# Optimization experiments

Hardware: AMD Instinct MI355X
Metric: run time of the kernel (lower is better)

## Reference

```python
import jax, jax.numpy as jnp
import numpy as np

N = 100000   # nodes
E = 800000   # edges
IN = 256     # input feature dim
H = 4        # heads per layer
D = 32       # per-head hidden dim (num_hidden)
SLOPE = 0.2  # leaky_relu negative slope


def setup_inputs() -> dict:
    key = jax.random.key(0)
    ks = jax.random.split(key, 8)
    s = 0.1  # weight scale for numerical stability
    x = jax.random.normal(ks[0], (N, IN), jnp.float32)
    edge_index = jax.random.randint(ks[1], (2, E), 0, N, dtype=jnp.int32)
    W0 = jax.random.normal(ks[2], (IN, H * D), jnp.float32) * s
    al0 = jax.random.normal(ks[3], (H, D), jnp.float32) * s
    ar0 = jax.random.normal(ks[4], (H, D), jnp.float32) * s
    W1 = jax.random.normal(ks[5], (H * D, H * D), jnp.float32) * s
    al1 = jax.random.normal(ks[6], (H, D), jnp.float32) * s
    ar1 = jax.random.normal(ks[7], (H, D), jnp.float32) * s
    return {"x": x, "edge_index": edge_index, "W0": W0, "al0": al0,
            "ar0": ar0, "W1": W1, "al1": al1, "ar1": ar1}


def _gat_layer(h, W, al, ar, src, dst, residual):
    """One GATConv: project, edge attention, dst-wise softmax, scatter-agg."""
    n = h.shape[0]
    feat = (h @ W).reshape(n, H, D)              # [N,H,D]
    el = jnp.einsum('nhd,hd->nh', feat, al)      # [N,H]
    er = jnp.einsum('nhd,hd->nh', feat, ar)      # [N,H]
    e = jax.nn.leaky_relu(el[src] + er[dst], SLOPE)   # raw scores [E,H]
    # edge softmax grouped by destination node (numerically stable)
    emax = jax.ops.segment_max(e, dst, num_segments=n)   # [N,H]
    eexp = jnp.exp(e - emax[dst])                          # [E,H]
    denom = jax.ops.segment_sum(eexp, dst, num_segments=n)  # [N,H]
    a = eexp / denom[dst]                                  # attention [E,H]
    msg = feat[src] * a[:, :, None]                        # [E,H,D]
    rst = jax.ops.segment_sum(msg, dst, num_segments=n)    # [N,H,D]
    if residual:
        rst = rst + h.reshape(n, H, D)  # identity residual (dims match)
    rst = jax.nn.elu(rst)               # activation
    return rst, a, e


def reference(x, edge_index, W0, al0, ar0, W1, al1, ar1):
    src, dst = edge_index[0], edge_index[1]
    # layer 0: no residual
    h1, a0, e0 = _gat_layer(x, W0, al0, ar0, src, dst, residual=False)
    atten0 = e0.mean(axis=-1)  # e_gat.flatten(1).mean(-1) -> [E]
    # layer 1: residual
    h2, a1, e1 = _gat_layer(h1.reshape(N, H * D), W1, al1, ar1, src, dst,
                            residual=True)
    atten1 = e1.mean(axis=-1)
    temp = h2.reshape(N, H * D)          # flattened node embeddings
    heads = tuple(h2[:, i] for i in range(H))  # per-head [N,D]
    return (temp,) + heads + (e1, atten0, atten1)
```

## Files before the change

### kernel.cpp

```cpp
#include <hip/hip_runtime.h>
#include <hip/hip_bf16.h>


typedef _Float16 f16;
typedef _Float16 f16x2 __attribute__((ext_vector_type(2)));
typedef _Float16 f16x8 __attribute__((ext_vector_type(8)));
typedef float f32x2 __attribute__((ext_vector_type(2)));
typedef float f32x4 __attribute__((ext_vector_type(4)));

__device__ __forceinline__ void gload16(const void* g, void* l) {
    __builtin_amdgcn_global_load_lds(
        (const __attribute__((address_space(1))) unsigned int*)g,
        (__attribute__((address_space(3))) unsigned int*)l, 16, 0, 0);
}

__global__ void prep(const float* __restrict__ W0, const float* __restrict__ W1,
                     f16* __restrict__ Wth0, f16* __restrict__ Wtl0,
                     f16* __restrict__ Wth1, f16* __restrict__ Wtl1,
                     const int* __restrict__ dsts, int* __restrict__ deg, int E) {
    int i = blockIdx.x * blockDim.x + threadIdx.x;
    if (i < 256 * 128) {
        int k = i >> 7, c = i & 127;
        float v = W0[i];
        f16 h = (f16)v;
        Wth0[(size_t)c * 256 + k] = h;
        Wtl0[(size_t)c * 256 + k] = (f16)(v - (float)h);
    } else if (i < 256 * 128 + 128 * 128) {
        int j = i - 256 * 128;
        int k = j >> 7, c = j & 127;
        float v = W1[j];
        f16 h = (f16)v;
        Wth1[(size_t)c * 128 + k] = h;
        Wtl1[(size_t)c * 128 + k] = (f16)(v - (float)h);
    } else {
        int e = i - (256 * 128 + 128 * 128);
        if (e < E) atomicAdd(&deg[dsts[e]], 1);
    }
}

template <int AFP16>
__device__ __forceinline__ void gemm_body(
        int bid, const void* __restrict__ Xv, const f16* __restrict__ Wth,
        const f16* __restrict__ Wtl, f16* __restrict__ Y16,
        const float* __restrict__ al, const float* __restrict__ ar,
        float* __restrict__ el_out, float* __restrict__ er_out,
        int nrows, int K) {
    __shared__ float As32[AFP16 ? 1 : 128 * 32];
    __shared__ f16   As16[AFP16 ? 128 * 32 : 1];
    __shared__ f16   Bh[128 * 32];
    __shared__ f16   Bl[128 * 32];
    const int t    = threadIdx.x;
    const int wave = t >> 6;
    const int lane = t & 63;
    const int lr   = lane & 15;
    const int kg   = lane >> 4;
    const int row0 = bid * 128;

    f32x4 acc[2][8];
    #pragma unroll
    for (int i = 0; i < 2; ++i)
        #pragma unroll
        for (int j = 0; j < 8; ++j) acc[i][j] = (f32x4){0.f, 0.f, 0.f, 0.f};

    for (int k0 = 0; k0 < K; k0 += 32) {
        if constexpr (!AFP16) {
            #pragma unroll
            for (int j = 0; j < 4; ++j) {
                int G = t + 256 * j;
                int row = G >> 3, slot = G & 7;
                int g = slot ^ (row & 7);
                int grow = row0 + row; if (grow >= nrows) grow = nrows - 1;
                gload16((const float*)Xv + (size_t)grow * K + k0 + g * 4,
                        &As32[G * 4]);
            }
        } else {
            #pragma unroll
            for (int j = 0; j < 2; ++j) {
                int G = t + 256 * j;
                int row = G >> 2, g4 = G & 3;
                int grow = row0 + row; if (grow >= nrows) grow = nrows - 1;
                gload16((const f16*)Xv + (size_t)grow * K + k0 + g4 * 8,
                        &As16[G * 8]);
            }
        }
        #pragma unroll
        for (int j = 0; j < 2; ++j) {
            int G = t + 256 * j;
            int r = G >> 2, g4 = G & 3;
            int p = ((r & 15) << 3) | (r >> 4);
            gload16(Wth + (size_t)p * K + k0 + g4 * 8, &Bh[G * 8]);
            gload16(Wtl + (size_t)p * K + k0 + g4 * 8, &Bl[G * 8]);
        }
        __syncthreads();

        const int ar0_ = wave * 32 + lr;
        f16x8 ah0, ah1, alo0, alo1;
        if constexpr (!AFP16) {
            int s0 = (2 * kg) ^ (lr & 7);
            int s1 = (2 * kg + 1) ^ (lr & 7);
            f32x4 u0 = *(const f32x4*)&As32[ar0_ * 32 + s0 * 4];
            f32x4 u1 = *(const f32x4*)&As32[ar0_ * 32 + s1 * 4];
            f32x4 v0 = *(const f32x4*)&As32[(ar0_ + 16) * 32 + s0 * 4];
            f32x4 v1 = *(const f32x4*)&As32[(ar0_ + 16) * 32 + s1 * 4];
            float a8[8] = {u0[0], u0[1], u0[2], u0[3], u1[0], u1[1], u1[2], u1[3]};
            float b8[8] = {v0[0], v0[1], v0[2], v0[3], v1[0], v1[1], v1[2], v1[3]};
            #pragma unroll
            for (int i = 0; i < 8; ++i) {
                f16 h0 = (f16)a8[i]; ah0[i] = h0; alo0[i] = (f16)(a8[i] - (float)h0);
                f16 h1 = (f16)b8[i]; ah1[i] = h1; alo1[i] = (f16)(b8[i] - (float)h1);
            }
        } else {
            ah0 = *(const f16x8*)&As16[ar0_ * 32 + kg * 8];
            ah1 = *(const f16x8*)&As16[(ar0_ + 16) * 32 + kg * 8];
        }
        f16x8 bh[8];
        #pragma unroll
        for (int cb = 0; cb < 8; ++cb)
            bh[cb] = *(const f16x8*)&Bh[(cb * 16 + lr) * 32 + kg * 8];

        #pragma unroll
        for (int cb = 0; cb < 8; ++cb) {
            acc[0][cb] = __builtin_amdgcn_mfma_f32_16x16x32_f16(ah0, bh[cb], acc[0][cb], 0, 0, 0);
            acc[1][cb] = __builtin_amdgcn_mfma_f32_16x16x32_f16(ah1, bh[cb], acc[1][cb], 0, 0, 0);
        }
        if constexpr (!AFP16) {
            #pragma unroll
            for (int cb = 0; cb < 8; ++cb) {
                acc[0][cb] = __builtin_amdgcn_mfma_f32_16x16x32_f16(alo0, bh[cb], acc[0][cb], 0, 0, 0);
                acc[1][cb] = __builtin_amdgcn_mfma_f32_16x16x32_f16(alo1, bh[cb], acc[1][cb], 0, 0, 0);
            }
        }
        #pragma unroll
        for (int cb = 0; cb < 8; ++cb) {
            f16x8 bl = *(const f16x8*)&Bl[(cb * 16 + lr) * 32 + kg * 8];
            acc[0][cb] = __builtin_amdgcn_mfma_f32_16x16x32_f16(ah0, bl, acc[0][cb], 0, 0, 0);
            acc[1][cb] = __builtin_amdgcn_mfma_f32_16x16x32_f16(ah1, bl, acc[1][cb], 0, 0, 0);
        }
        __syncthreads();
    }

    const int hh = lr >> 2;
    const int co = (lr & 3) * 8;
    float alv[8], arv[8];
    #pragma unroll
    for (int j = 0; j < 8; ++j) {
        alv[j] = al[hh * 32 + co + j];
        arv[j] = ar[hh * 32 + co + j];
    }
    #pragma unroll
    for (int rb = 0; rb < 2; ++rb) {
        int rbase = row0 + wave * 32 + rb * 16 + kg * 4;
        #pragma unroll
        for (int r = 0; r < 4; ++r) {
            int grow = rbase + r;
            f16x8 hv;
            float sl_ = 0.0f, sr_ = 0.0f;
            #pragma unroll
            for (int cb = 0; cb < 8; ++cb) {
                float v = acc[rb][cb][r];
                hv[cb] = (f16)v;
                sl_ += v * alv[cb];
                sr_ += v * arv[cb];
            }
            sl_ += __shfl_xor(sl_, 1); sl_ += __shfl_xor(sl_, 2);
            sr_ += __shfl_xor(sr_, 1); sr_ += __shfl_xor(sr_, 2);
            if (grow < nrows) {
                *(f16x8*)(Y16 + (size_t)grow * 128 + lr * 8) = hv;
                if ((lane & 3) == 0) {
                    el_out[4 * (size_t)grow + hh] = sl_;
                    er_out[4 * (size_t)grow + hh] = sr_;
                }
            }
        }
    }
}

__device__ __forceinline__ void scan_body(int b, const int* __restrict__ deg,
                                          int* __restrict__ excl,
                                          int* __restrict__ bsums, int n) {
    __shared__ int wsums[4];
    int t = threadIdx.x;
    int base = b * 1024;
    int idx = base + t * 4;
    int v[4];
    #pragma unroll
    for (int i = 0; i < 4; ++i) v[i] = (idx + i < n) ? deg[idx + i] : 0;
    int tsum = v[0] + v[1] + v[2] + v[3];
    int lane = t & 63, wid = t >> 6;
    int incl = tsum;
    #pragma unroll
    for (int off = 1; off < 64; off <<= 1) {
        int u = __shfl_up(incl, off, 64);
        if (lane >= off) incl += u;
    }
    if (lane == 63) wsums[wid] = incl;
    __syncthreads();
    if (t == 0) {
        int s = 0;
        #pragma unroll
        for (int w = 0; w < 4; ++w) { int x = wsums[w]; wsums[w] = s; s += x; }
    }
    __syncthreads();
    int ex = incl - tsum + wsums[wid];
    int run = ex;
    #pragma unroll
    for (int i = 0; i < 4; ++i) { if (idx + i < n) excl[idx + i] = run; run += v[i]; }
    if (t == 255) bsums[b] = ex + tsum;
}

__global__ __launch_bounds__(256, 2) void gemm0_scan(
        const float* __restrict__ X, const f16* __restrict__ Wth,
        const f16* __restrict__ Wtl, f16* __restrict__ Y16,
        const float* __restrict__ al, const float* __restrict__ ar,
        float* __restrict__ el_out, float* __restrict__ er_out,
        int nrows, int K, int gblocks,
        const int* __restrict__ deg, int* __restrict__ excl,
        int* __restrict__ bsums, int n) {
    if ((int)blockIdx.x < gblocks)
        gemm_body<0>(blockIdx.x, X, Wth, Wtl, Y16, al, ar, el_out, er_out, nrows, K);
    else
        scan_body(blockIdx.x - gblocks, deg, excl, bsums, n);
}

__global__ __launch_bounds__(256, 2) void gemm_mfma1(
        const f16* __restrict__ X, const f16* __restrict__ Wth,
        const f16* __restrict__ Wtl, f16* __restrict__ Y16,
        const float* __restrict__ al, const float* __restrict__ ar,
        float* __restrict__ el_out, float* __restrict__ er_out,
        int nrows, int K) {
    gemm_body<1>(blockIdx.x, X, Wth, Wtl, Y16, al, ar, el_out, er_out, nrows, K);
}

__global__ __launch_bounds__(256) void scan_fin(int* __restrict__ row_off,
                                                const int* __restrict__ bsums,
                                                int* __restrict__ cursor,
                                                const int* __restrict__ deg,
                                                int n, int nb) {
    __shared__ int spfx;
    int b = blockIdx.x;
    int t = threadIdx.x;
    if (t < 64) {
        int v = 0;
        if (t < b && t < nb) v = bsums[t];
        int t2 = t + 64;
        if (t2 < b && t2 < nb) v += bsums[t2];
        #pragma unroll
        for (int off = 32; off; off >>= 1) v += __shfl_xor(v, off, 64);
        if (t == 0) spfx = v;
    }
    __syncthreads();
    int pfx = spfx;
    int base = b * 1024 + t * 4;
    #pragma unroll
    for (int i2 = 0; i2 < 4; ++i2) {
        int i = base + i2;
        if (i < n) {
            int v = row_off[i] + pfx;
            row_off[i] = v;
            cursor[i]  = v;
            if (i == n - 1) row_off[n] = v + deg[i];
        }
    }
}

__global__ void fill_csr_edge0(const int* __restrict__ srcs, const int* __restrict__ dsts,
                               int* __restrict__ cursor, int* __restrict__ csr_src,
                               const float* __restrict__ el, const float* __restrict__ er,
                               float* __restrict__ atten0, int E) {
    int e = blockIdx.x * blockDim.x + threadIdx.x;
    if (e >= E) return;
    int s = srcs[e], d = dsts[e];
    int p = atomicAdd(&cursor[d], 1);
    csr_src[p] = s;
    float4 elv = *(const float4*)(el + 4 * (size_t)s);
    float4 erv = *(const float4*)(er + 4 * (size_t)d);
    float v0 = elv.x + erv.x, v1 = elv.y + erv.y;
    float v2 = elv.z + erv.z, v3 = elv.w + erv.w;
    v0 = v0 > 0.0f ? v0 : 0.2f * v0;
    v1 = v1 > 0.0f ? v1 : 0.2f * v1;
    v2 = v2 > 0.0f ? v2 : 0.2f * v2;
    v3 = v3 > 0.0f ? v3 : 0.2f * v3;
    __builtin_nontemporal_store((v0 + v1 + v2 + v3) * 0.25f, atten0 + e);
}

__device__ __forceinline__ void edge1_body(int bid,
        const int* __restrict__ srcs, const int* __restrict__ dsts,
        const float* __restrict__ el, const float* __restrict__ er,
        float* __restrict__ e1_out, float* __restrict__ atten1, int E) {
    int e = bid * 256 + threadIdx.x;
    if (e >= E) return;
    int s = srcs[e], d = dsts[e];
    float4 elv = *(const float4*)(el + 4 * (size_t)s);
    float4 erv = *(const float4*)(er + 4 * (size_t)d);
    float v0 = elv.x + erv.x, v1 = elv.y + erv.y;
    float v2 = elv.z + erv.z, v3 = elv.w + erv.w;
    v0 = v0 > 0.0f ? v0 : 0.2f * v0;
    v1 = v1 > 0.0f ? v1 : 0.2f * v1;
    v2 = v2 > 0.0f ? v2 : 0.2f * v2;
    v3 = v3 > 0.0f ? v3 : 0.2f * v3;
    __builtin_nontemporal_store((f32x4){v0, v1, v2, v3},
                                (f32x4*)(e1_out + 4 * (size_t)e));
    __builtin_nontemporal_store((v0 + v1 + v2 + v3) * 0.25f, atten1 + e);
}

template <int LAYER>
__device__ __forceinline__ void agg_body(int bid,
        const int* __restrict__ row_off, const int* __restrict__ csr_src,
        const float* __restrict__ el, const float* __restrict__ er,
        const f16* __restrict__ feat16, const f16* __restrict__ resid16,
        f16* __restrict__ out16, float* __restrict__ out32,
        float* __restrict__ heads, int N) {
    int wave = (bid * 256 + (int)threadIdx.x) >> 6;
    if (wave >= N) return;
    int lane = threadIdx.x & 63;
    int q  = lane >> 4;
    int sc = lane & 15;
    int h  = sc >> 2;
    int start = row_off[wave];
    int dc    = row_off[wave + 1] - start;
    float er_h = er[4 * (size_t)wave + h];

    float acc[8];
    #pragma unroll
    for (int j = 0; j < 8; ++j) acc[j] = 0.0f;
    float dh = 0.0f;

    for (int cs = 0; cs < dc; cs += 64) {
        int act = dc - cs; if (act > 64) act = 64;
        int sl = (lane < act) ? csr_src[start + cs + lane] : 0;
        int i = 0;
        for (; i + 8 <= act; i += 8) {
            int s0 = __shfl(sl, i + q);
            int s1 = __shfl(sl, i + 4 + q);
            float x0 = el[4 * (size_t)s0 + h] + er_h;
            float x1 = el[4 * (size_t)s1 + h] + er_h;
            x0 = x0 > 0.0f ? x0 : 0.2f * x0;
            x1 = x1 > 0.0f ? x1 : 0.2f * x1;
            float w0 = __expf(x0);
            float w1 = __expf(x1);
            f16x8 f0 = *(const f16x8*)(feat16 + 128 * (size_t)s0 + sc * 8);
            f16x8 f1 = *(const f16x8*)(feat16 + 128 * (size_t)s1 + sc * 8);
            #pragma unroll
            for (int j = 0; j < 8; ++j) acc[j] += w0 * (float)f0[j];
            #pragma unroll
            for (int j = 0; j < 8; ++j) acc[j] += w1 * (float)f1[j];
            dh += w0 + w1;
        }
        for (; i < act; i += 4) {
            int e = i + q;
            bool on = e < act;
            int s = __shfl(sl, on ? e : 0);
            float x = el[4 * (size_t)s + h] + er_h;
            x = x > 0.0f ? x : 0.2f * x;
            float w = on ? __expf(x) : 0.0f;
            f16x8 fv = *(const f16x8*)(feat16 + 128 * (size_t)s + sc * 8);
            #pragma unroll
            for (int j = 0; j < 8; ++j) acc[j] += w * (float)fv[j];
            dh += w;
        }
    }

    #pragma unroll
    for (int j = 0; j < 8; ++j) {
        acc[j] += __shfl_xor(acc[j], 16);
        acc[j] += __shfl_xor(acc[j], 32);
    }
    dh += __shfl_xor(dh, 16);
    dh += __shfl_xor(dh, 32);

    float inv = (dc > 0) ? 1.0f / dh : 0.0f;
    float ax = (q == 0) ? acc[0] : (q == 1) ? acc[2] : (q == 2) ? acc[4] : acc[6];
    float ay = (q == 0) ? acc[1] : (q == 1) ? acc[3] : (q == 2) ? acc[5] : acc[7];
    ax *= inv; ay *= inv;
    int c0 = sc * 8 + q * 2;
    size_t o = 128 * (size_t)wave + c0;
    if (LAYER == 1) {
        f16x2 rv = *(const f16x2*)(resid16 + o);
        ax += (float)rv[0]; ay += (float)rv[1];
    }
    ax = ax > 0.0f ? ax : __expf(ax) - 1.0f;
    ay = ay > 0.0f ? ay : __expf(ay) - 1.0f;
    if (LAYER == 0) {
        f16x2 hv; hv[0] = (f16)ax; hv[1] = (f16)ay;
        *(f16x2*)(out16 + o) = hv;
    } else {
        __builtin_nontemporal_store((f32x2){ax, ay}, (f32x2*)(out32 + o));
        __builtin_nontemporal_store(
            (f32x2){ax, ay},
            (f32x2*)(heads + (size_t)h * N * 32 + (size_t)wave * 32 + (c0 & 31)));
    }
}

__global__ __launch_bounds__(256) void aggregate0(const int* __restrict__ row_off,
                                                  const int* __restrict__ csr_src,
                                                  const float* __restrict__ el,
                                                  const float* __restrict__ er,
                                                  const f16* __restrict__ feat16,
                                                  f16* __restrict__ out16, int N) {
    agg_body<0>(blockIdx.x, row_off, csr_src, el, er, feat16, nullptr,
                out16, nullptr, nullptr, N);
}

__global__ __launch_bounds__(256) void layer1_fused(
        const int* __restrict__ row_off, const int* __restrict__ csr_src,
        const float* __restrict__ el, const float* __restrict__ er,
        const f16* __restrict__ feat16, const f16* __restrict__ resid16,
        float* __restrict__ out32, float* __restrict__ heads,
        const int* __restrict__ srcs, const int* __restrict__ dsts,
        float* __restrict__ e1_out, float* __restrict__ atten1,
        int aggBlocks, int N, int E) {
    if ((int)blockIdx.x < aggBlocks)
        agg_body<1>(blockIdx.x, row_off, csr_src, el, er, feat16, resid16,
                    nullptr, out32, heads, N);
    else
        edge1_body(blockIdx.x - aggBlocks, srcs, dsts, el, er, e1_out, atten1, E);
}

extern "C" void kernel_launch(void* const* d_in, const int* in_sizes, int n_in,
                              void* d_out, int out_size, void* d_ws, size_t ws_size,
                              hipStream_t stream) {
    const float* x   = (const float*)d_in[0];
    const int*   ei  = (const int*)d_in[1];
    const float* W0  = (const float*)d_in[2];
    const float* al0 = (const float*)d_in[3];
    const float* ar0 = (const float*)d_in[4];
    const float* W1  = (const float*)d_in[5];
    const float* al1 = (const float*)d_in[6];
    const float* ar1 = (const float*)d_in[7];

    const int N = in_sizes[0] / 256;
    const int E = in_sizes[1] / 2;
    const size_t NF = (size_t)N * 128;

    const int* srcs = ei;
    const int* dsts = ei + E;

    float* out = (float*)d_out;
    f16*   f16ws  = (f16*)d_ws;
    f16*   feat16 = f16ws;
    f16*   h1_16  = feat16 + NF;
    float* el   = (float*)(h1_16 + NF);
    float* er   = el + (size_t)N * 4;
    f16*   wth0 = (f16*)(er + (size_t)N * 4);
    f16*   wtl0 = wth0 + (size_t)128 * 256;
    f16*   wth1 = wtl0 + (size_t)128 * 256;
    f16*   wtl1 = wth1 + (size_t)128 * 128;
    int*   ints    = (int*)(wtl1 + (size_t)128 * 128);
    int*   deg     = ints;
    int*   row_off = deg + N;
    int*   cursor  = row_off + N + 1;
    int*   csr_src = cursor + N;
    int*   bsums   = csr_src + E;

    float* heads      = out + NF;
    float* e1_out     = out + 2 * NF;
    float* atten0_out = e1_out + (size_t)E * 4;
    float* atten1_out = atten0_out + E;

    hipMemsetAsync(deg, 0, (size_t)N * sizeof(int), stream);
    const int wtot = 256 * 128 + 128 * 128;
    prep<<<(wtot + E + 255) / 256, 256, 0, stream>>>(W0, W1, wth0, wtl0, wth1, wtl1,
                                                     dsts, deg, E);

    const int gemm_blocks = (N + 127) / 128;
    const int agg_blocks  = (N + 3) / 4;
    const int edge_blocks = (E + 255) / 256;
    const int nb = (N + 1023) / 1024;

    gemm0_scan<<<gemm_blocks + nb, 256, 0, stream>>>(x, wth0, wtl0, feat16, al0, ar0,
                                                     el, er, N, 256, gemm_blocks,
                                                     deg, row_off, bsums, N);
    scan_fin<<<nb, 256, 0, stream>>>(row_off, bsums, cursor, deg, N, nb);
    fill_csr_edge0<<<edge_blocks, 256, 0, stream>>>(srcs, dsts, cursor, csr_src,
                                                    el, er, atten0_out, E);
    aggregate0<<<agg_blocks, 256, 0, stream>>>(row_off, csr_src, el, er,
                                               feat16, h1_16, N);

    gemm_mfma1<<<gemm_blocks, 256, 0, stream>>>(h1_16, wth1, wtl1, feat16, al1, ar1,
                                                el, er, N, 128);
    layer1_fused<<<agg_blocks + edge_blocks, 256, 0, stream>>>(
        row_off, csr_src, el, er, feat16, h1_16, out, heads,
        srcs, dsts, e1_out, atten1_out, agg_blocks, N, E);
}
```

Before: 416.2 us.

## Process two nodes per wave in aggregation and drop A-low split MFMA pass

The aggregation kernel now assigns each half-wave (32 lanes) to one destination node instead of a full wave per node. It handles 2 edges per step per half, reduces across 2 quarter groups, and writes 4-wide vectorized outputs. This targets lane underuse on low-degree nodes, and the launch uses half as many blocks. Separately, the layer-0 GEMM no longer computes the fp16 low-residual of the fp32 input A. That removes one third of its MFMAs at the cost of reduced accuracy in the projection.

Result: faster. 406.1 us (-2.4%).

```diff
diff --git a/kernel.cpp b/kernel.cpp
--- a/kernel.cpp
+++ b/kernel.cpp
@@ -4,6 +4,7 @@
 
 typedef _Float16 f16;
 typedef _Float16 f16x2 __attribute__((ext_vector_type(2)));
+typedef _Float16 f16x4 __attribute__((ext_vector_type(4)));
 typedef _Float16 f16x8 __attribute__((ext_vector_type(8)));
 typedef float f32x2 __attribute__((ext_vector_type(2)));
 typedef float f32x4 __attribute__((ext_vector_type(4)));
@@ -94,7 +95,7 @@
         __syncthreads();
 
         const int ar0_ = wave * 32 + lr;
-        f16x8 ah0, ah1, alo0, alo1;
+        f16x8 ah0, ah1;
         if constexpr (!AFP16) {
             int s0 = (2 * kg) ^ (lr & 7);
             int s1 = (2 * kg + 1) ^ (lr & 7);
@@ -106,8 +107,8 @@
             float b8[8] = {v0[0], v0[1], v0[2], v0[3], v1[0], v1[1], v1[2], v1[3]};
             #pragma unroll
             for (int i = 0; i < 8; ++i) {
-                f16 h0 = (f16)a8[i]; ah0[i] = h0; alo0[i] = (f16)(a8[i] - (float)h0);
-                f16 h1 = (f16)b8[i]; ah1[i] = h1; alo1[i] = (f16)(b8[i] - (float)h1);
+                ah0[i] = (f16)a8[i];
+                ah1[i] = (f16)b8[i];
             }
         } else {
             ah0 = *(const f16x8*)&As16[ar0_ * 32 + kg * 8];
@@ -122,13 +123,6 @@
         for (int cb = 0; cb < 8; ++cb) {
             acc[0][cb] = __builtin_amdgcn_mfma_f32_16x16x32_f16(ah0, bh[cb], acc[0][cb], 0, 0, 0);
             acc[1][cb] = __builtin_amdgcn_mfma_f32_16x16x32_f16(ah1, bh[cb], acc[1][cb], 0, 0, 0);
-        }
-        if constexpr (!AFP16) {
-            #pragma unroll
-            for (int cb = 0; cb < 8; ++cb) {
-                acc[0][cb] = __builtin_amdgcn_mfma_f32_16x16x32_f16(alo0, bh[cb], acc[0][cb], 0, 0, 0);
-                acc[1][cb] = __builtin_amdgcn_mfma_f32_16x16x32_f16(alo1, bh[cb], acc[1][cb], 0, 0, 0);
-            }
         }
         #pragma unroll
         for (int cb = 0; cb < 8; ++cb) {
@@ -310,28 +304,33 @@
         const f16* __restrict__ feat16, const f16* __restrict__ resid16,
         f16* __restrict__ out16, float* __restrict__ out32,
         float* __restrict__ heads, int N) {
-    int wave = (bid * 256 + (int)threadIdx.x) >> 6;
-    if (wave >= N) return;
+    int wv   = (bid * 256 + (int)threadIdx.x) >> 6;
     int lane = threadIdx.x & 63;
-    int q  = lane >> 4;
+    int half = lane >> 5;
+    int node = wv * 2 + half;
+    int l31  = lane & 31;
+    int q2 = (lane >> 4) & 1;
     int sc = lane & 15;
     int h  = sc >> 2;
-    int start = row_off[wave];
-    int dc    = row_off[wave + 1] - start;
-    float er_h = er[4 * (size_t)wave + h];
+    bool valid = node < N;
+    int nclamp = valid ? node : N - 1;
+    int start = row_off[nclamp];
+    int dc    = valid ? (row_off[nclamp + 1] - start) : 0;
+    float er_h = er[4 * (size_t)nclamp + h];
 
     float acc[8];
     #pragma unroll
     for (int j = 0; j < 8; ++j) acc[j] = 0.0f;
     float dh = 0.0f;
-
-    for (int cs = 0; cs < dc; cs += 64) {
-        int act = dc - cs; if (act > 64) act = 64;
-        int sl = (lane < act) ? csr_src[start + cs + lane] : 0;
+    const int base = half << 5;
+
+    for (int cs = 0; cs < dc; cs += 32) {
+        int act = dc - cs; if (act > 32) act = 32;
+        int sl = (l31 < act) ? csr_src[start + cs + l31] : 0;
         int i = 0;
-        for (; i + 8 <= act; i += 8) {
-            int s0 = __shfl(sl, i + q);
-            int s1 = __shfl(sl, i + 4 + q);
+        for (; i + 4 <= act; i += 4) {
+            int s0 = __shfl(sl, base + i + q2);
+            int s1 = __shfl(sl, base + i + 2 + q2);
             float x0 = el[4 * (size_t)s0 + h] + er_h;
             float x1 = el[4 * (size_t)s1 + h] + er_h;
             x0 = x0 > 0.0f ? x0 : 0.2f * x0;
@@ -346,10 +345,10 @@
             for (int j = 0; j < 8; ++j) acc[j] += w1 * (float)f1[j];
             dh += w0 + w1;
         }
-        for (; i < act; i += 4) {
-            int e = i + q;
+        for (; i < act; i += 2) {
+            int e = i + q2;
             bool on = e < act;
-            int s = __shfl(sl, on ? e : 0);
+            int s = __shfl(sl, base + (on ? e : 0));
             float x = el[4 * (size_t)s + h] + er_h;
             x = x > 0.0f ? x : 0.2f * x;
             float w = on ? __expf(x) : 0.0f;
@@ -361,33 +360,34 @@
     }
 
     #pragma unroll
-    for (int j = 0; j < 8; ++j) {
-        acc[j] += __shfl_xor(acc[j], 16);
-        acc[j] += __shfl_xor(acc[j], 32);
-    }
+    for (int j = 0; j < 8; ++j) acc[j] += __shfl_xor(acc[j], 16);
     dh += __shfl_xor(dh, 16);
-    dh += __shfl_xor(dh, 32);
+    if (!valid) return;
 
     float inv = (dc > 0) ? 1.0f / dh : 0.0f;
-    float ax = (q == 0) ? acc[0] : (q == 1) ? acc[2] : (q == 2) ? acc[4] : acc[6];
-    float ay = (q == 0) ? acc[1] : (q == 1) ? acc[3] : (q == 2) ? acc[5] : acc[7];
-    ax *= inv; ay *= inv;
-    int c0 = sc * 8 + q * 2;
-    size_t o = 128 * (size_t)wave + c0;
+    float r0 = (q2 ? acc[4] : acc[0]) * inv;
+    float r1 = (q2 ? acc[5] : acc[1]) * inv;
+    float r2 = (q2 ? acc[6] : acc[2]) * inv;
+    float r3 = (q2 ? acc[7] : acc[3]) * inv;
+    int c0 = sc * 8 + q2 * 4;
+    size_t o = 128 * (size_t)node + c0;
     if (LAYER == 1) {
-        f16x2 rv = *(const f16x2*)(resid16 + o);
-        ax += (float)rv[0]; ay += (float)rv[1];
-    }
-    ax = ax > 0.0f ? ax : __expf(ax) - 1.0f;
-    ay = ay > 0.0f ? ay : __expf(ay) - 1.0f;
+        f16x4 rv = *(const f16x4*)(resid16 + o);
+        r0 += (float)rv[0]; r1 += (float)rv[1];
+        r2 += (float)rv[2]; r3 += (float)rv[3];
+    }
+    r0 = r0 > 0.0f ? r0 : __expf(r0) - 1.0f;
+    r1 = r1 > 0.0f ? r1 : __expf(r1) - 1.0f;
+    r2 = r2 > 0.0f ? r2 : __expf(r2) - 1.0f;
+    r3 = r3 > 0.0f ? r3 : __expf(r3) - 1.0f;
     if (LAYER == 0) {
-        f16x2 hv; hv[0] = (f16)ax; hv[1] = (f16)ay;
-        *(f16x2*)(out16 + o) = hv;
+        f16x4 hv; hv[0] = (f16)r0; hv[1] = (f16)r1; hv[2] = (f16)r2; hv[3] = (f16)r3;
+        *(f16x4*)(out16 + o) = hv;
     } else {
-        __builtin_nontemporal_store((f32x2){ax, ay}, (f32x2*)(out32 + o));
+        __builtin_nontemporal_store((f32x4){r0, r1, r2, r3}, (f32x4*)(out32 + o));
         __builtin_nontemporal_store(
-            (f32x2){ax, ay},
-            (f32x2*)(heads + (size_t)h * N * 32 + (size_t)wave * 32 + (c0 & 31)));
+            (f32x4){r0, r1, r2, r3},
+            (f32x4*)(heads + (size_t)h * N * 32 + (size_t)node * 32 + (c0 & 31)));
     }
 }
 
@@ -463,7 +463,7 @@
                                                      dsts, deg, E);
 
     const int gemm_blocks = (N + 127) / 128;
-    const int agg_blocks  = (N + 3) / 4;
+    const int agg_blocks  = (N + 7) / 8;
     const int edge_blocks = (E + 255) / 256;
     const int nb = (N + 1023) / 1024;
 
```
